# Kernel optimization log

Measured on AMD Instinct MI355X. Metric: run time of the kernel, lower is better.

The kernel has to match this reference:

```python
import jax, jax.numpy as jnp
import numpy as np

N_QUBITS = 10
N_LAYERS = 4


def setup_inputs() -> dict:
    key = jax.random.key(0)
    k1, k2 = jax.random.split(key)
    x = jax.random.normal(k1, (4, 1024, 64), dtype=jnp.float32)
    params = jax.random.normal(k2, (N_LAYERS, N_QUBITS), dtype=jnp.float32)
    return {"x": x, "params": params}


def _apply_ry(state, q, theta):
    # state: [N] + [2]*n (wire 0 is the most-significant axis, PennyLane convention)
    # theta: scalar (shared angle) or [N] (per-sample angle)
    theta = jnp.asarray(theta)
    c = jnp.cos(theta * 0.5)
    s = jnp.sin(theta * 0.5)
    if theta.ndim == 1:  # per-sample angle -> broadcast over the qubit axes
        shp = (-1,) + (1,) * (state.ndim - 2)
        c = c.reshape(shp)
        s = s.reshape(shp)
    s0 = jax.lax.index_in_dim(state, 0, axis=q + 1, keepdims=False)
    s1 = jax.lax.index_in_dim(state, 1, axis=q + 1, keepdims=False)
    # RY = [[cos, -sin], [sin, cos]] (real matrix -> state stays real)
    return jnp.stack([c * s0 - s * s1, s * s0 + c * s1], axis=q + 1)


def _apply_cnot(state, ctrl, tgt):
    a0 = jax.lax.index_in_dim(state, 0, axis=ctrl + 1, keepdims=False)
    a1 = jax.lax.index_in_dim(state, 1, axis=ctrl + 1, keepdims=False)
    # after removing the control axis, axes beyond it shift down by one
    t_axis = tgt + 1 if tgt < ctrl else tgt
    a1 = jnp.flip(a1, axis=t_axis)  # X on target within the control=1 slab
    return jnp.stack([a0, a1], axis=ctrl + 1)


def reference(x, params):
    B, T, H = x.shape
    L, n = params.shape
    N = B * T
    xf = x.reshape(N, H)[:, :n]  # encoding angles, [N, n]
    # initial |0...0> statevector, batched over all B*T tokens
    state = jnp.zeros((N, 2 ** n), dtype=x.dtype).at[:, 0].set(1.0)
    state = state.reshape((N,) + (2,) * n)
    for l in range(L):
        for q in range(n):
            state = _apply_ry(state, q, params[l, q])
        for q in range(n - 1):
            state = _apply_cnot(state, q, q + 1)
        state = _apply_cnot(state, n - 1, 0)
    for q in range(n):
        state = _apply_ry(state, q, xf[:, q])
    probs = state * state  # real amplitudes -> |amp|^2
    z = []
    for q in range(n):
        axes = tuple(a for a in range(1, n + 1) if a != q + 1)
        p = probs.sum(axis=axes)  # [N, 2]
        z.append(p[:, 0] - p[:, 1])  # <Z_q> = P(0) - P(1)
    out = jnp.stack(z, axis=-1).reshape(B, T, n)
    if H > n:
        out = jnp.concatenate([out, jnp.zeros((B, T, H - n), dtype=out.dtype)], axis=-1)
    return out
```

## Files before the change

### kernel.cpp

```cpp
#include <hip/hip_runtime.h>
#include <math.h>

#define NQ 10
#define NL 4

__global__ __launch_bounds__(256) void qc_fused(const float* __restrict__ x,
                                                const float* __restrict__ params,
                                                float* __restrict__ out) {
    __shared__ float sA[NQ];
    __shared__ float sB[NQ];
    __shared__ float csc[NL * NQ];
    __shared__ float css[NL * NQ];
    __shared__ float perm_buf[1024];

    const int tid = threadIdx.x;

    if (tid < 64) {
        const int lane = tid;
        if (lane < NL * NQ) {
            float sv, cv;
            sincosf(0.5f * params[lane], &sv, &cv);
            csc[lane] = cv;
            css[lane] = sv;
        }
        __asm__ volatile("s_waitcnt lgkmcnt(0)" ::: "memory");

        int pidx[16];
#pragma unroll
        for (int r = 0; r < 16; ++r) {
            int t = lane * 16 + r;
            t ^= (t & 1) << 9;
#pragma unroll
            for (int j = 8; j >= 0; --j)
                t ^= ((t >> (9 - j)) & 1) << (8 - j);
            pidx[r] = (t & 15) * 64 + (t >> 4);
        }

        float v[16];
#pragma unroll
        for (int r = 0; r < 16; ++r) v[r] = 0.0f;
        if (lane == 0) v[0] = 1.0f;

#pragma unroll
        for (int l = 0; l < NL; ++l) {
#pragma unroll
            for (int q = 0; q < 6; ++q) {
                const float c = csc[l * NQ + q];
                const float s = css[l * NQ + q];
                const float t = ((lane >> (5 - q)) & 1) ? s : -s;
#pragma unroll
                for (int r = 0; r < 16; ++r) {
                    const float p = __shfl_xor(v[r], 1 << (5 - q), 64);
                    v[r] = fmaf(t, p, c * v[r]);
                }
            }
#pragma unroll
            for (int q = 6; q < NQ; ++q) {
                const float c = csc[l * NQ + q];
                const float s = css[l * NQ + q];
                const int mr = 1 << (9 - q);
#pragma unroll
                for (int r = 0; r < 16; ++r) {
                    if (!(r & mr)) {
                        const float v0 = v[r], v1 = v[r | mr];
                        v[r]      = fmaf(-s, v1, c * v0);
                        v[r | mr] = fmaf( s, v0, c * v1);
                    }
                }
            }
#pragma unroll
            for (int r = 0; r < 16; ++r) perm_buf[r * 64 + lane] = v[r];
            __asm__ volatile("s_waitcnt lgkmcnt(0)" ::: "memory");
#pragma unroll
            for (int r = 0; r < 16; ++r) v[r] = perm_buf[pidx[r]];
            __asm__ volatile("s_waitcnt lgkmcnt(0)" ::: "memory");
        }

        float E = 0.0f;
#pragma unroll
        for (int r = 0; r < 16; ++r) E = fmaf(v[r], v[r], E);

        float pA[NQ], pB[NQ];
#pragma unroll
        for (int q = 0; q < 6; ++q) {
            float b = 0.0f;
#pragma unroll
            for (int r = 0; r < 16; ++r) {
                const float p = __shfl_xor(v[r], 1 << (5 - q), 64);
                b = fmaf(v[r], p, b);
            }
            pA[q] = ((lane >> (5 - q)) & 1) ? -E : E;
            pB[q] = b;
        }
#pragma unroll
        for (int q = 6; q < NQ; ++q) {
            const int mr = 1 << (9 - q);
            float a = 0.0f, b = 0.0f;
#pragma unroll
            for (int r = 0; r < 16; ++r) {
                a += ((r & mr) ? -1.0f : 1.0f) * v[r] * v[r];
                b = fmaf(v[r], v[r ^ mr], b);
            }
            pA[q] = a;
            pB[q] = b;
        }
#pragma unroll
        for (int q = 0; q < NQ; ++q) {
            float a = pA[q], b = pB[q];
#pragma unroll
            for (int off = 32; off > 0; off >>= 1) {
                a += __shfl_xor(a, off, 64);
                b += __shfl_xor(b, off, 64);
            }
            if (lane == 0) { sA[q] = a; sB[q] = b; }
        }
    }
    __syncthreads();

    const int i = blockIdx.x * 256 + tid;
    const int h0 = (i << 2) & 63;
    float4 o = make_float4(0.f, 0.f, 0.f, 0.f);
    if (h0 < 12) {
        const float4 xv = reinterpret_cast<const float4*>(x)[i];
        float sv, cv;
        sincosf(xv.x, &sv, &cv); o.x = cv * sA[h0]     - sv * sB[h0];
        sincosf(xv.y, &sv, &cv); o.y = cv * sA[h0 + 1] - sv * sB[h0 + 1];
        if (h0 + 2 < NQ) {
            sincosf(xv.z, &sv, &cv); o.z = cv * sA[h0 + 2] - sv * sB[h0 + 2];
            sincosf(xv.w, &sv, &cv); o.w = cv * sA[h0 + 3] - sv * sB[h0 + 3];
        }
    }
    reinterpret_cast<float4*>(out)[i] = o;
}

extern "C" void kernel_launch(void* const* d_in, const int* in_sizes, int n_in,
                              void* d_out, int out_size, void* d_ws, size_t ws_size,
                              hipStream_t stream) {
    const float* x      = (const float*)d_in[0];
    const float* params = (const float*)d_in[1];
    float* out = (float*)d_out;

    const int total4 = out_size / 4;
    qc_fused<<<total4 / 256, 256, 0, stream>>>(x, params, out);
}
```

Baseline: 64.36 us.

## Overlap x loads with statevector sim, use bpermute and LDS reduction

Moves the x load and sincos of encoding angles before the first wave's statevector simulation, so the other waves' global loads overlap with it. Replaces the LDS scatter/gather permutation with a closed-form ds_bpermute, and replaces the per-qubit shuffle reductions with an LDS transpose-and-sum by 20 lanes. It also switches to fast __sincosf intrinsics, which trades some accuracy for lower latency.

```diff
diff --git a/kernel.cpp b/kernel.cpp
--- a/kernel.cpp
+++ b/kernel.cpp
@@ -7,39 +7,48 @@
 __global__ __launch_bounds__(256) void qc_fused(const float* __restrict__ x,
                                                 const float* __restrict__ params,
                                                 float* __restrict__ out) {
-    __shared__ float sA[NQ];
-    __shared__ float sB[NQ];
     __shared__ float csc[NL * NQ];
     __shared__ float css[NL * NQ];
-    __shared__ float perm_buf[1024];
+    __shared__ __align__(16) float red[20][68];
+    __shared__ float sAB[20];
 
     const int tid = threadIdx.x;
+    const int i = blockIdx.x * 256 + tid;
+    const int h0 = (i << 2) & 63;
+    const bool act = (h0 < 12);
+
+    float c0 = 0.f, s0 = 0.f, c1 = 0.f, s1 = 0.f;
+    float c2 = 0.f, s2 = 0.f, c3 = 0.f, s3 = 0.f;
+    if (act) {
+        const float4 xv = reinterpret_cast<const float4*>(x)[i];
+        __sincosf(xv.x, &s0, &c0);
+        __sincosf(xv.y, &s1, &c1);
+        if (h0 + 2 < NQ) {
+            __sincosf(xv.z, &s2, &c2);
+            __sincosf(xv.w, &s3, &c3);
+        }
+    }
 
     if (tid < 64) {
         const int lane = tid;
         if (lane < NL * NQ) {
             float sv, cv;
-            sincosf(0.5f * params[lane], &sv, &cv);
+            __sincosf(0.5f * params[lane], &sv, &cv);
             csc[lane] = cv;
             css[lane] = sv;
         }
-        __asm__ volatile("s_waitcnt lgkmcnt(0)" ::: "memory");
 
-        int pidx[16];
-#pragma unroll
-        for (int r = 0; r < 16; ++r) {
-            int t = lane * 16 + r;
-            t ^= (t & 1) << 9;
-#pragma unroll
-            for (int j = 8; j >= 0; --j)
-                t ^= ((t >> (9 - j)) & 1) << (8 - j);
-            pidx[r] = (t & 15) * 64 + (t >> 4);
-        }
+        const int lam = ((lane ^ (lane >> 1)) & 31) | (lane & 32);
+        const int addr_even = lam << 2;
+        const int addr_odd  = (lam ^ 48) << 2;
+        const int par = __builtin_popcount(lane) & 1;
 
         float v[16];
 #pragma unroll
         for (int r = 0; r < 16; ++r) v[r] = 0.0f;
         if (lane == 0) v[0] = 1.0f;
+
+        __asm__ volatile("s_waitcnt lgkmcnt(0)" ::: "memory");
 
 #pragma unroll
         for (int l = 0; l < NL; ++l) {
@@ -68,29 +77,34 @@
                     }
                 }
             }
+            float nv[16];
 #pragma unroll
-            for (int r = 0; r < 16; ++r) perm_buf[r * 64 + lane] = v[r];
-            __asm__ volatile("s_waitcnt lgkmcnt(0)" ::: "memory");
+            for (int r = 0; r < 16; ++r) {
+                const int gsrc = ((r ^ (r >> 1)) & 7) | (r & 8);
+                const float u = par ? v[gsrc ^ 8] : v[gsrc];
+                nv[r] = __int_as_float(__builtin_amdgcn_ds_bpermute(
+                    (r & 1) ? addr_odd : addr_even, __float_as_int(u)));
+            }
 #pragma unroll
-            for (int r = 0; r < 16; ++r) v[r] = perm_buf[pidx[r]];
-            __asm__ volatile("s_waitcnt lgkmcnt(0)" ::: "memory");
+            for (int r = 0; r < 16; ++r) v[r] = nv[r];
         }
 
         float E = 0.0f;
 #pragma unroll
         for (int r = 0; r < 16; ++r) E = fmaf(v[r], v[r], E);
 
-        float pA[NQ], pB[NQ];
 #pragma unroll
         for (int q = 0; q < 6; ++q) {
-            float b = 0.0f;
+            const int m = 1 << (5 - q);
+            float b = 0.0f, b2 = 0.0f;
 #pragma unroll
             for (int r = 0; r < 16; ++r) {
-                const float p = __shfl_xor(v[r], 1 << (5 - q), 64);
-                b = fmaf(v[r], p, b);
+                const float p = __shfl_xor(v[r], m, 64);
+                if (r & 1) b2 = fmaf(v[r], p, b2);
+                else       b  = fmaf(v[r], p, b);
             }
-            pA[q] = ((lane >> (5 - q)) & 1) ? -E : E;
-            pB[q] = b;
+            red[q][lane]      = ((lane >> (5 - q)) & 1) ? -E : E;
+            red[10 + q][lane] = b + b2;
         }
 #pragma unroll
         for (int q = 6; q < NQ; ++q) {
@@ -101,33 +115,32 @@
                 a += ((r & mr) ? -1.0f : 1.0f) * v[r] * v[r];
                 b = fmaf(v[r], v[r ^ mr], b);
             }
-            pA[q] = a;
-            pB[q] = b;
+            red[q][lane]      = a;
+            red[10 + q][lane] = b;
         }
+        __asm__ volatile("s_waitcnt lgkmcnt(0)" ::: "memory");
+
+        if (lane < 20) {
+            const float4* row = reinterpret_cast<const float4*>(&red[lane][0]);
+            float4 a = row[0], b = row[1];
 #pragma unroll
-        for (int q = 0; q < NQ; ++q) {
-            float a = pA[q], b = pB[q];
-#pragma unroll
-            for (int off = 32; off > 0; off >>= 1) {
-                a += __shfl_xor(a, off, 64);
-                b += __shfl_xor(b, off, 64);
+            for (int j = 2; j < 16; j += 2) {
+                const float4 ra = row[j], rb = row[j + 1];
+                a.x += ra.x; a.y += ra.y; a.z += ra.z; a.w += ra.w;
+                b.x += rb.x; b.y += rb.y; b.z += rb.z; b.w += rb.w;
             }
-            if (lane == 0) { sA[q] = a; sB[q] = b; }
+            sAB[lane] = (a.x + a.y) + (a.z + a.w) + (b.x + b.y) + (b.z + b.w);
         }
     }
     __syncthreads();
 
-    const int i = blockIdx.x * 256 + tid;
-    const int h0 = (i << 2) & 63;
     float4 o = make_float4(0.f, 0.f, 0.f, 0.f);
-    if (h0 < 12) {
-        const float4 xv = reinterpret_cast<const float4*>(x)[i];
-        float sv, cv;
-        sincosf(xv.x, &sv, &cv); o.x = cv * sA[h0]     - sv * sB[h0];
-        sincosf(xv.y, &sv, &cv); o.y = cv * sA[h0 + 1] - sv * sB[h0 + 1];
+    if (act) {
+        o.x = c0 * sAB[h0]     - s0 * sAB[10 + h0];
+        o.y = c1 * sAB[h0 + 1] - s1 * sAB[10 + h0 + 1];
         if (h0 + 2 < NQ) {
-            sincosf(xv.z, &sv, &cv); o.z = cv * sA[h0 + 2] - sv * sB[h0 + 2];
-            sincosf(xv.w, &sv, &cv); o.w = cv * sA[h0 + 3] - sv * sB[h0 + 3];
+            o.z = c2 * sAB[h0 + 2] - s2 * sAB[10 + h0 + 2];
+            o.w = c3 * sAB[h0 + 3] - s3 * sAB[10 + h0 + 3];
         }
     }
     reinterpret_cast<float4*>(out)[i] = o;
```

After: 69.93 us. +8.6%, slower.
